# Optimization experiments

Hardware: AMD Instinct MI355X
Metric: run time of the kernel (lower is better)

Reference implementation:

```python
import jax, jax.numpy as jnp
import numpy as np

NUM_USERS, NUM_ITEMS, NUM_GROUPS = 100000, 50000, 20000
D = 64
B, M = 16384, 50


def setup_inputs() -> dict:
    key = jax.random.key(0)
    ks = jax.random.split(key, 16)
    inp = {
        "group_inputs": jax.random.randint(ks[0], (B,), 0, NUM_GROUPS),
        "item_inputs": jax.random.randint(ks[1], (B,), 0, NUM_ITEMS),
        "member_ids": jax.random.randint(ks[2], (B, M), 0, NUM_USERS),
        "member_lengths": jax.random.randint(ks[3], (B,), 0, M),
        # embedding tables (xavier-ish scale)
        "user_table": jax.random.normal(ks[4], (NUM_USERS, D), jnp.float32) * 0.05,
        "item_table": jax.random.normal(ks[5], (NUM_ITEMS, D), jnp.float32) * 0.05,
        "group_table": jax.random.normal(ks[6], (NUM_GROUPS, D), jnp.float32) * 0.05,
        # attention MLP: 2D -> 16 -> 1
        "att_w1": jax.random.normal(ks[7], (2 * D, 16), jnp.float32) * 0.1,
        "att_b1": jnp.zeros((16,), jnp.float32),
        "att_w2": jax.random.normal(ks[8], (16, 1), jnp.float32) * 0.1,
        "att_b2": jnp.zeros((1,), jnp.float32),
        # predict MLP: 3D -> 8 -> 1
        "pred_w1": jax.random.normal(ks[9], (3 * D, 8), jnp.float32) * 0.1,
        "pred_b1": jnp.zeros((8,), jnp.float32),
        "pred_w2": jax.random.normal(ks[10], (8, 1), jnp.float32) * 0.1,
        "pred_b2": jnp.zeros((1,), jnp.float32),
    }
    return inp


def reference(group_inputs, item_inputs, member_ids, member_lengths,
              user_table, item_table, group_table,
              att_w1, att_b1, att_w2, att_b2,
              pred_w1, pred_b1, pred_w2, pred_b2):
    # mask: at least one valid member per group
    mask = jnp.arange(M)[None, :] <= member_lengths[:, None]          # [B, M] bool
    mem_e = user_table[member_ids]                                    # [B, M, D]
    item_e = item_table[item_inputs]                                  # [B, D]

    # attention over members: concat(member, item) -> 16 -> 1
    gi = jnp.concatenate(
        [mem_e, jnp.broadcast_to(item_e[:, None, :], mem_e.shape)], axis=-1)  # [B, M, 2D]
    h = jax.nn.relu(jnp.einsum('bmk,kh->bmh', gi, att_w1) + att_b1)   # [B, M, 16]
    scores = (jnp.einsum('bmh,ho->bmo', h, att_w2) + att_b2)[..., 0]  # [B, M]
    scores = jnp.where(mask, scores, -jnp.inf)
    at_wt = jax.nn.softmax(scores, axis=-1)                           # [B, M]

    g_att = jnp.einsum('bm,bmd->bd', at_wt, mem_e)                    # [B, D]
    g = g_att + group_table[group_inputs]                             # [B, D]

    elem = g * item_e
    new_e = jnp.concatenate([elem, g, item_e], axis=-1)               # [B, 3D]
    ph = jax.nn.relu(new_e @ pred_w1 + pred_b1)                       # [B, 8]
    y = jax.nn.sigmoid(ph @ pred_w2 + pred_b2)                        # [B, 1]
    return y
```

## Files before the change

### kernel.cpp

```cpp
#include <hip/hip_runtime.h>
#include <math.h>

constexpr int MM = 50;
constexpr int DD = 64;
constexpr int HH = 16;
constexpr int PH = 8;

__global__ __launch_bounds__(256) void precompute_kernel(
    const float* __restrict__ user_table,
    const float* __restrict__ item_table,
    const int*   __restrict__ item_inputs,
    const float* __restrict__ att_w1,
    const float* __restrict__ att_b1,
    float* __restrict__ U,
    float* __restrict__ Ib,
    int nU, int B, int userBlocks)
{
    const bool isU = (int)blockIdx.x < userBlocks;
    const float4* rp;
    const float*  w1;
    float* dst;
    float acc[HH];

    if (isU) {
        const int row = (int)blockIdx.x * 256 + (int)threadIdx.x;
        if (row >= nU) return;
        rp  = (const float4*)(user_table + (size_t)row * DD);
        w1  = att_w1;
        dst = U + (size_t)row * HH;
        #pragma unroll
        for (int j = 0; j < HH; ++j) acc[j] = 0.0f;
    } else {
        const int r = ((int)blockIdx.x - userBlocks) * 256 + (int)threadIdx.x;
        if (r >= B) return;
        const int item = item_inputs[r];
        rp  = (const float4*)(item_table + (size_t)item * DD);
        w1  = att_w1 + (size_t)DD * HH;
        dst = Ib + (size_t)r * HH;
        #pragma unroll
        for (int j = 0; j < HH; ++j) acc[j] = att_b1[j];
    }

    #pragma unroll 4
    for (int d4 = 0; d4 < DD / 4; ++d4) {
        const float4 x = rp[d4];
        const float* w = w1 + (size_t)(d4 * 4) * HH;
        #pragma unroll
        for (int j = 0; j < HH; ++j) {
            acc[j] = fmaf(x.x, w[0 * HH + j], acc[j]);
            acc[j] = fmaf(x.y, w[1 * HH + j], acc[j]);
            acc[j] = fmaf(x.z, w[2 * HH + j], acc[j]);
            acc[j] = fmaf(x.w, w[3 * HH + j], acc[j]);
        }
    }

    float4* o4 = (float4*)dst;
    o4[0] = make_float4(acc[0],  acc[1],  acc[2],  acc[3]);
    o4[1] = make_float4(acc[4],  acc[5],  acc[6],  acc[7]);
    o4[2] = make_float4(acc[8],  acc[9],  acc[10], acc[11]);
    o4[3] = make_float4(acc[12], acc[13], acc[14], acc[15]);
}

__global__ __launch_bounds__(256) void agree_block(
    const int* __restrict__ group_inputs,
    const int* __restrict__ item_inputs,
    const int* __restrict__ member_ids,
    const int* __restrict__ member_lengths,
    const float* __restrict__ user_table,
    const float* __restrict__ item_table,
    const float* __restrict__ group_table,
    const float* __restrict__ att_w2,
    const float* __restrict__ att_b2,
    const float* __restrict__ pred_w1,
    const float* __restrict__ pred_b1,
    const float* __restrict__ pred_w2,
    const float* __restrict__ pred_b2,
    const float* __restrict__ U,
    const float* __restrict__ Ib,
    float* __restrict__ out)
{
    __shared__ float lds_part[3][DD];

    const int lane = threadIdx.x & 63;
    const int wv   = threadIdx.x >> 6;
    const int b    = blockIdx.x;

    const int my_m  = (lane < MM) ? lane : (MM - 1);
    const int my_id = member_ids[b * MM + my_m];
    const int len   = member_lengths[b];
    const int item_idx = item_inputs[b];
    const int gid      = group_inputs[b];

    const float4* up = (const float4*)(U + (size_t)my_id * HH);
    const float4 u0 = up[0], u1 = up[1], u2 = up[2], u3 = up[3];
    const float* ib = Ib + (size_t)b * HH;

    float score = att_b2[0];
    {
        const float uu[HH] = { u0.x,u0.y,u0.z,u0.w, u1.x,u1.y,u1.z,u1.w,
                               u2.x,u2.y,u2.z,u2.w, u3.x,u3.y,u3.z,u3.w };
        #pragma unroll
        for (int j = 0; j < HH; ++j)
            score = fmaf(fmaxf(uu[j] + ib[j], 0.0f), att_w2[j], score);
    }

    const bool valid = (lane < MM) && (lane <= len);
    score = valid ? score : -INFINITY;

    float mx = score;
    #pragma unroll
    for (int off = 32; off > 0; off >>= 1) mx = fmaxf(mx, __shfl_xor(mx, off, 64));
    const float e = valid ? __expf(score - mx) : 0.0f;
    float sum = e;
    #pragma unroll
    for (int off = 32; off > 0; off >>= 1) sum += __shfl_xor(sum, off, 64);
    const float wnorm = e / sum;

    const float item_d = item_table[(size_t)item_idx * DD + lane];
    const float grp_d  = group_table[(size_t)gid * DD + lane];

    const int mcnt = (len < MM - 1 ? len : MM - 1) + 1;
    float gw = 0.0f;
    {
        float w[7]; int id[7]; float x[7];
        #pragma unroll
        for (int k = 0; k < 7; ++k) {
            const int m = wv + 4 * k;
            w[k]  = __shfl(wnorm, m, 64);
            id[k] = __shfl(my_id, m, 64);
        }
        #pragma unroll
        for (int k = 0; k < 7; ++k)
            x[k] = user_table[(size_t)id[k] * DD + lane];
        #pragma unroll
        for (int k = 0; k < 7; ++k) gw = fmaf(w[k], x[k], gw);
    }
    if (wv + 28 < mcnt) {
        float w[6]; int id[6]; float x[6];
        #pragma unroll
        for (int k = 0; k < 6; ++k) {
            const int m = wv + 4 * (k + 7);
            w[k]  = __shfl(wnorm, m, 64);
            id[k] = __shfl(my_id, m, 64);
        }
        #pragma unroll
        for (int k = 0; k < 6; ++k)
            x[k] = user_table[(size_t)id[k] * DD + lane];
        #pragma unroll
        for (int k = 0; k < 6; ++k) gw = fmaf(w[k], x[k], gw);
    }

    if (wv) lds_part[wv - 1][lane] = gw;
    __syncthreads();
    if (wv) return;

    float g = gw + lds_part[0][lane] + lds_part[1][lane] + lds_part[2][lane];
    g += grp_d;

    const float elem = g * item_d;
    float p[PH];
    {
        const float* pa = pred_w1 + (size_t)lane * PH;
        const float* pb = pred_w1 + (size_t)(DD + lane) * PH;
        const float* pc = pred_w1 + (size_t)(2 * DD + lane) * PH;
        #pragma unroll
        for (int j = 0; j < PH; ++j)
            p[j] = fmaf(elem, pa[j], fmaf(g, pb[j], item_d * pc[j]));
    }
    #pragma unroll
    for (int off = 32; off > 0; off >>= 1) {
        #pragma unroll
        for (int j = 0; j < PH; ++j) p[j] += __shfl_xor(p[j], off, 64);
    }

    if (lane == 0) {
        float acc = pred_b2[0];
        #pragma unroll
        for (int j = 0; j < PH; ++j)
            acc = fmaf(fmaxf(p[j] + pred_b1[j], 0.0f), pred_w2[j], acc);
        out[b] = 1.0f / (1.0f + __expf(-acc));
    }
}

__global__ __launch_bounds__(256) void agree_fallback(
    const int* __restrict__ group_inputs,
    const int* __restrict__ item_inputs,
    const int* __restrict__ member_ids,
    const int* __restrict__ member_lengths,
    const float* __restrict__ user_table,
    const float* __restrict__ item_table,
    const float* __restrict__ group_table,
    const float* __restrict__ att_w1,
    const float* __restrict__ att_b1,
    const float* __restrict__ att_w2,
    const float* __restrict__ att_b2,
    const float* __restrict__ pred_w1,
    const float* __restrict__ pred_b1,
    const float* __restrict__ pred_w2,
    const float* __restrict__ pred_b2,
    float* __restrict__ out,
    int B)
{
    __shared__ float lds_wt[4][MM];
    __shared__ int   lds_id[4][MM];

    const int lane = threadIdx.x & 63;
    const int wave = threadIdx.x >> 6;
    const int b = blockIdx.x * 4 + wave;
    if (b >= B) return;

    const int my_m = (lane < MM) ? lane : (MM - 1);
    const int my_id = member_ids[b * MM + my_m];
    if (lane < MM) lds_id[wave][lane] = my_id;

    const int item_idx = item_inputs[b];
    const float item_d = item_table[(size_t)item_idx * DD + lane];

    float h[HH];
    {
        const float* w1row = att_w1 + (size_t)(DD + lane) * HH;
        #pragma unroll
        for (int j = 0; j < HH; ++j) h[j] = item_d * w1row[j];
        #pragma unroll
        for (int off = 32; off > 0; off >>= 1) {
            #pragma unroll
            for (int j = 0; j < HH; ++j) h[j] += __shfl_xor(h[j], off, 64);
        }
        #pragma unroll
        for (int j = 0; j < HH; ++j) h[j] += att_b1[j];
    }

    const float* myrow = user_table + (size_t)my_id * DD;
    #pragma unroll 4
    for (int d4 = 0; d4 < DD / 4; ++d4) {
        const float4 x = ((const float4*)myrow)[d4];
        const float* w1d = att_w1 + (size_t)(d4 * 4) * HH;
        #pragma unroll
        for (int j = 0; j < HH; ++j) {
            h[j] = fmaf(x.x, w1d[0 * HH + j], h[j]);
            h[j] = fmaf(x.y, w1d[1 * HH + j], h[j]);
            h[j] = fmaf(x.z, w1d[2 * HH + j], h[j]);
            h[j] = fmaf(x.w, w1d[3 * HH + j], h[j]);
        }
    }

    float score = att_b2[0];
    #pragma unroll
    for (int j = 0; j < HH; ++j) score = fmaf(fmaxf(h[j], 0.0f), att_w2[j], score);

    const int len = member_lengths[b];
    const bool valid = (lane < MM) && (lane <= len);
    score = valid ? score : -INFINITY;

    float mx = score;
    #pragma unroll
    for (int off = 32; off > 0; off >>= 1) mx = fmaxf(mx, __shfl_xor(mx, off, 64));
    float e = valid ? __expf(score - mx) : 0.0f;
    float sum = e;
    #pragma unroll
    for (int off = 32; off > 0; off >>= 1) sum += __shfl_xor(sum, off, 64);
    if (lane < MM) lds_wt[wave][lane] = e / sum;
    __builtin_amdgcn_s_waitcnt(0);

    const int mcnt = (len < MM - 1 ? len : MM - 1) + 1;
    float g = 0.0f;
    #pragma unroll 2
    for (int m = 0; m < mcnt; ++m) {
        g = fmaf(lds_wt[wave][m],
                 user_table[(size_t)lds_id[wave][m] * DD + lane], g);
    }
    const int gid = group_inputs[b];
    g += group_table[(size_t)gid * DD + lane];

    const float elem = g * item_d;
    float p[PH];
    {
        const float* pa = pred_w1 + (size_t)lane * PH;
        const float* pb = pred_w1 + (size_t)(DD + lane) * PH;
        const float* pc = pred_w1 + (size_t)(2 * DD + lane) * PH;
        #pragma unroll
        for (int j = 0; j < PH; ++j)
            p[j] = fmaf(elem, pa[j], fmaf(g, pb[j], item_d * pc[j]));
    }
    #pragma unroll
    for (int off = 32; off > 0; off >>= 1) {
        #pragma unroll
        for (int j = 0; j < PH; ++j) p[j] += __shfl_xor(p[j], off, 64);
    }

    if (lane == 0) {
        float acc = pred_b2[0];
        #pragma unroll
        for (int j = 0; j < PH; ++j)
            acc = fmaf(fmaxf(p[j] + pred_b1[j], 0.0f), pred_w2[j], acc);
        out[b] = 1.0f / (1.0f + __expf(-acc));
    }
}

extern "C" void kernel_launch(void* const* d_in, const int* in_sizes, int n_in,
                              void* d_out, int out_size, void* d_ws, size_t ws_size,
                              hipStream_t stream) {
    const int*   group_inputs   = (const int*)d_in[0];
    const int*   item_inputs    = (const int*)d_in[1];
    const int*   member_ids     = (const int*)d_in[2];
    const int*   member_lengths = (const int*)d_in[3];
    const float* user_table     = (const float*)d_in[4];
    const float* item_table     = (const float*)d_in[5];
    const float* group_table    = (const float*)d_in[6];
    const float* att_w1         = (const float*)d_in[7];
    const float* att_b1         = (const float*)d_in[8];
    const float* att_w2         = (const float*)d_in[9];
    const float* att_b2         = (const float*)d_in[10];
    const float* pred_w1        = (const float*)d_in[11];
    const float* pred_b1        = (const float*)d_in[12];
    const float* pred_w2        = (const float*)d_in[13];
    const float* pred_b2        = (const float*)d_in[14];
    float* out = (float*)d_out;

    const int B  = in_sizes[0];
    const int nU = in_sizes[4] / DD;
    const size_t need = ((size_t)nU + (size_t)B) * HH * sizeof(float);

    if (ws_size >= need) {
        float* U  = (float*)d_ws;
        float* Ib = U + (size_t)nU * HH;
        const int userBlocks = (nU + 255) / 256;
        const int itemBlocks = (B + 255) / 256;
        precompute_kernel<<<userBlocks + itemBlocks, 256, 0, stream>>>(
            user_table, item_table, item_inputs, att_w1, att_b1,
            U, Ib, nU, B, userBlocks);
        agree_block<<<B, 256, 0, stream>>>(
            group_inputs, item_inputs, member_ids, member_lengths,
            user_table, item_table, group_table,
            att_w2, att_b2, pred_w1, pred_b1, pred_w2, pred_b2,
            U, Ib, out);
    } else {
        const int blocks = (B + 3) / 4;
        agree_fallback<<<blocks, 256, 0, stream>>>(
            group_inputs, item_inputs, member_ids, member_lengths,
            user_table, item_table, group_table,
            att_w1, att_b1, att_w2, att_b2,
            pred_w1, pred_b1, pred_w2, pred_b2,
            out, B);
    }
}
```

Before: 150.9 us.

## Process one group per wave and stage member weights and ids in LDS

The main kernel changes from one 256-thread block per group, which split members across four waves and reduced through LDS with a barrier, to one group per wave with four groups per block. Member weights and ids are written to a per-wave LDS buffer and read back in chunks of eight, replacing the shuffles. The loop runs only over valid members, so padded members are no longer loaded. This removes the block barrier and cross-wave reduction, at the cost of fewer loads in flight per group, since each group's gather loop is now serial within one wave. It also relies on a waitcnt instead of a barrier for LDS visibility within the wave and uses 32-bit unsigned index arithmetic.

```diff
diff --git a/kernel.cpp b/kernel.cpp
--- a/kernel.cpp
+++ b/kernel.cpp
@@ -5,6 +5,8 @@
 constexpr int DD = 64;
 constexpr int HH = 16;
 constexpr int PH = 8;
+constexpr int WAVES_PER_BLOCK = 4;
+constexpr int SLOTS = 56;
 
 __global__ __launch_bounds__(256) void precompute_kernel(
     const float* __restrict__ user_table,
@@ -61,7 +63,7 @@
     o4[3] = make_float4(acc[12], acc[13], acc[14], acc[15]);
 }
 
-__global__ __launch_bounds__(256) void agree_block(
+__global__ __launch_bounds__(256) void agree_main(
     const int* __restrict__ group_inputs,
     const int* __restrict__ item_inputs,
     const int* __restrict__ member_ids,
@@ -77,13 +79,15 @@
     const float* __restrict__ pred_b2,
     const float* __restrict__ U,
     const float* __restrict__ Ib,
-    float* __restrict__ out)
+    float* __restrict__ out,
+    int B)
 {
-    __shared__ float lds_part[3][DD];
+    __shared__ float2 pairs[WAVES_PER_BLOCK][SLOTS];
 
     const int lane = threadIdx.x & 63;
     const int wv   = threadIdx.x >> 6;
-    const int b    = blockIdx.x;
+    const int b    = blockIdx.x * WAVES_PER_BLOCK + wv;
+    if (b >= B) return;
 
     const int my_m  = (lane < MM) ? lane : (MM - 1);
     const int my_id = member_ids[b * MM + my_m];
@@ -91,7 +95,10 @@
     const int item_idx = item_inputs[b];
     const int gid      = group_inputs[b];
 
-    const float4* up = (const float4*)(U + (size_t)my_id * HH);
+    const float item_d = item_table[(unsigned)(item_idx * DD + lane)];
+    const float grp_d  = group_table[(unsigned)(gid * DD + lane)];
+
+    const float4* up = (const float4*)(U + ((size_t)(unsigned)my_id * HH));
     const float4 u0 = up[0], u1 = up[1], u2 = up[2], u3 = up[3];
     const float* ib = Ib + (size_t)b * HH;
 
@@ -116,45 +123,26 @@
     for (int off = 32; off > 0; off >>= 1) sum += __shfl_xor(sum, off, 64);
     const float wnorm = e / sum;
 
-    const float item_d = item_table[(size_t)item_idx * DD + lane];
-    const float grp_d  = group_table[(size_t)gid * DD + lane];
-
-    const int mcnt = (len < MM - 1 ? len : MM - 1) + 1;
-    float gw = 0.0f;
-    {
-        float w[7]; int id[7]; float x[7];
-        #pragma unroll
-        for (int k = 0; k < 7; ++k) {
-            const int m = wv + 4 * k;
-            w[k]  = __shfl(wnorm, m, 64);
-            id[k] = __shfl(my_id, m, 64);
+    if (lane < SLOTS) pairs[wv][lane] = make_float2(wnorm, __int_as_float(my_id));
+    __builtin_amdgcn_s_waitcnt(0);
+
+    const int mcnt   = (len < MM - 1 ? len : MM - 1) + 1;
+    const int chunks = (mcnt + 7) >> 3;
+
+    float g = 0.0f;
+    for (int c = 0; c < chunks; ++c) {
+        float2 q[8];
+        #pragma unroll
+        for (int k = 0; k < 8; ++k) q[k] = pairs[wv][c * 8 + k];
+        float x[8];
+        #pragma unroll
+        for (int k = 0; k < 8; ++k) {
+            const unsigned idx = (unsigned)(__float_as_int(q[k].y) * DD + lane);
+            x[k] = user_table[idx];
         }
         #pragma unroll
-        for (int k = 0; k < 7; ++k)
-            x[k] = user_table[(size_t)id[k] * DD + lane];
-        #pragma unroll
-        for (int k = 0; k < 7; ++k) gw = fmaf(w[k], x[k], gw);
-    }
-    if (wv + 28 < mcnt) {
-        float w[6]; int id[6]; float x[6];
-        #pragma unroll
-        for (int k = 0; k < 6; ++k) {
-            const int m = wv + 4 * (k + 7);
-            w[k]  = __shfl(wnorm, m, 64);
-            id[k] = __shfl(my_id, m, 64);
-        }
-        #pragma unroll
-        for (int k = 0; k < 6; ++k)
-            x[k] = user_table[(size_t)id[k] * DD + lane];
-        #pragma unroll
-        for (int k = 0; k < 6; ++k) gw = fmaf(w[k], x[k], gw);
-    }
-
-    if (wv) lds_part[wv - 1][lane] = gw;
-    __syncthreads();
-    if (wv) return;
-
-    float g = gw + lds_part[0][lane] + lds_part[1][lane] + lds_part[2][lane];
+        for (int k = 0; k < 8; ++k) g = fmaf(q[k].x, x[k], g);
+    }
     g += grp_d;
 
     const float elem = g * item_d;
@@ -320,6 +308,7 @@
     const int B  = in_sizes[0];
     const int nU = in_sizes[4] / DD;
     const size_t need = ((size_t)nU + (size_t)B) * HH * sizeof(float);
+    const int blocks = (B + WAVES_PER_BLOCK - 1) / WAVES_PER_BLOCK;
 
     if (ws_size >= need) {
         float* U  = (float*)d_ws;
@@ -329,13 +318,12 @@
         precompute_kernel<<<userBlocks + itemBlocks, 256, 0, stream>>>(
             user_table, item_table, item_inputs, att_w1, att_b1,
             U, Ib, nU, B, userBlocks);
-        agree_block<<<B, 256, 0, stream>>>(
+        agree_main<<<blocks, 256, 0, stream>>>(
             group_inputs, item_inputs, member_ids, member_lengths,
             user_table, item_table, group_table,
             att_w2, att_b2, pred_w1, pred_b1, pred_w2, pred_b2,
-            U, Ib, out);
+            U, Ib, out, B);
     } else {
-        const int blocks = (B + 3) / 4;
         agree_fallback<<<blocks, 256, 0, stream>>>(
             group_inputs, item_inputs, member_ids, member_lengths,
             user_table, item_table, group_table,
```

After: 146.0 us. -3.2%, faster.
